# Performance work log

Hardware: AMD Instinct MI355X
Metric: run time of the kernel (lower is better)

## Reference

```python
import jax, jax.numpy as jnp
import numpy as np


def _pad_kernel_like(kernel_oc0, H, W, ks):
    # torch: F.pad(k,(p,p,p,p)) then if shape mismatch F.pad(k,(0,1,0,1))
    p = (H - ks) // 2
    extra = H - (ks + 2 * p)  # 0 or 1
    return jnp.pad(kernel_oc0, ((0, 0), (p, p + extra), (p, p + extra)))


def setup_inputs() -> dict:
    key = jax.random.key(0)
    k1, k2 = jax.random.split(key)
    B, C, H, W = 8, 16, 128, 128
    O, KS = 32, 9
    x = jax.random.normal(k1, (B, C, H, W), dtype=jnp.float32)
    # kaiming_uniform-ish init scale
    fan_in = C * KS * KS
    bound = float(np.sqrt(6.0 / fan_in))
    kernel = jax.random.uniform(k2, (O, C, KS, KS), dtype=jnp.float32,
                                minval=-bound, maxval=bound)
    return {"x": x, "kernel": kernel}


def reference(x, kernel):
    # x: [B,C,H,W] float32, kernel: [O,C,ks,ks] float32
    B, C, H, W = x.shape
    O, ks = kernel.shape[0], kernel.shape[-1]
    # Faithful to original bug: only kernel[:, 0] is used for every input channel.
    k = _pad_kernel_like(kernel[:, 0], H, W, ks)  # [O,H,W]
    # 4f optical FFT convolution: ifftshift -> FFT -> multiply -> IFFT -> fftshift -> |.|
    Fx = jnp.fft.fft2(jnp.fft.ifftshift(x, axes=(-2, -1)))   # [B,C,H,W] complex64
    Fk = jnp.fft.fft2(jnp.fft.ifftshift(k, axes=(-2, -1)))   # [O,H,W]   complex64
    prod = Fx[:, None, :, :, :] * Fk[None, :, None, :, :]    # [B,O,C,H,W]
    field = jnp.fft.fftshift(jnp.fft.ifft2(prod), axes=(-2, -1))
    out_pc = jnp.abs(field)                                  # per-(out,in)-channel intensity
    return out_pc.sum(axis=2)                                # [B,O,H,W]
```

## Files before the change

### kernel.cpp

```cpp
#include <hip/hip_runtime.h>


typedef __attribute__((ext_vector_type(8)))  short  short8;
typedef __attribute__((ext_vector_type(4)))  float  float4v;
typedef __attribute__((ext_vector_type(4)))  unsigned int uint4v;

#define NROW 11
#define NCC  144
#define CHSZ (NROW * NCC)
#define NSLOT (16 * NROW * 72)

__device__ __forceinline__ unsigned short f2bf(float f) {
    union { float f; unsigned int u; } a; a.f = f;
    unsigned int u = a.u;
    u += 0x7fffu + ((u >> 16) & 1u);
    return (unsigned short)(u >> 16);
}

#define MFMA_PHASE(q_, odd_, Bf_, Dv_)                                       \
    {                                                                        \
        uint4v fr;                                                           \
        if (odd_) {                                                          \
            fr.x = (unsigned int)((((unsigned long long)wnd[(q_)+1] << 32) | wnd[(q_)+0]) >> 16); \
            fr.y = (unsigned int)((((unsigned long long)wnd[(q_)+2] << 32) | wnd[(q_)+1]) >> 16); \
            fr.z = (unsigned int)((((unsigned long long)wnd[(q_)+3] << 32) | wnd[(q_)+2]) >> 16); \
            fr.w = (unsigned int)((((unsigned long long)wnd[(q_)+4] << 32) | wnd[(q_)+3]) >> 16); \
        } else {                                                             \
            fr.x = wnd[(q_)+0]; fr.y = wnd[(q_)+1];                          \
            fr.z = wnd[(q_)+2]; fr.w = wnd[(q_)+3];                          \
        }                                                                    \
        short8 af = __builtin_bit_cast(short8, fr);                          \
        Dv_ = __builtin_amdgcn_mfma_f32_16x16x32_bf16(af, Bf_, Dv_, 0, 0, 0); \
    }

#define LOAD_SLOT(s_, v0_, v1_, ad_)                                         \
    {                                                                        \
        int ch  = (s_) / 792;                                                \
        int rem = (s_) - 792 * ch;                                           \
        int rr  = rem / 72;                                                  \
        int ccd = rem - 72 * rr;                                             \
        int cc  = 2 * ccd;                                                   \
        int xrow = (i0 - 4 + rr) & 127;                                      \
        const float* xp = xb + (ch << 14) + (xrow << 7);                     \
        v0_ = xp[(132 - cc) & 127];                                          \
        v1_ = xp[(131 - cc) & 127];                                          \
        ad_ = ch * CHSZ + rr * NCC + cc;                                     \
    }

__global__ __launch_bounds__(512, 4)
void optical_conv_69698729279498(const float* __restrict__ x,
                                 const float* __restrict__ kern,
                                 float* __restrict__ out) {
    __shared__ __align__(16) unsigned short ldsb[16 * CHSZ];

    const int tid = threadIdx.x;
    const int l   = tid & 63;
    const int w   = tid >> 6;
    const int h   = w & 1;
    const int oh  = (w >> 1) & 1;
    const int rh  = w >> 2;
    const int i0  = blockIdx.x * 2;
    const int b   = blockIdx.y;

    const int lk   = l & 15;
    const int g    = (l >> 4) & 1;
    const int hi32 = l >> 5;
    const int g2   = l >> 4;
    const int o    = oh * 16 + lk;

    const float* xb = x + ((size_t)b << 18);

    float v0a[13], v1a[13]; int aa[13];
#pragma unroll
    for (int k = 0; k < 13; ++k) {
        int s = tid + 512 * k;
        LOAD_SLOT(s, v0a[k], v1a[k], aa[k]);
    }
    float v0b[12], v1b[12]; int ab[12];
#pragma unroll
    for (int k = 0; k < 12; ++k) {
        int s = tid + 512 * (13 + k);
        if (s > NSLOT - 1) s = NSLOT - 1;
        LOAD_SLOT(s, v0b[k], v1b[k], ab[k]);
    }
#pragma unroll
    for (int k = 0; k < 13; ++k) {
        unsigned int pk2 = (unsigned int)f2bf(v0a[k]) | ((unsigned int)f2bf(v1a[k]) << 16);
        *(unsigned int*)&ldsb[aa[k]] = pk2;
    }
#pragma unroll
    for (int k = 0; k < 12; ++k) {
        unsigned int pk2 = (unsigned int)f2bf(v0b[k]) | ((unsigned int)f2bf(v1b[k]) << 16);
        *(unsigned int*)&ldsb[ab[k]] = pk2;
    }

    short8 Bf[5];
#pragma unroll
    for (int ck = 0; ck < 5; ++ck) {
        const int ti  = 2 * ck + (g2 >> 1);
        const int tj0 = (g2 & 1) * 8;
        unsigned int pk[4];
#pragma unroll
        for (int ee = 0; ee < 4; ++ee) {
            int tj_a = tj0 + 2 * ee, tj_b = tj_a + 1;
            float va = (ti <= 8 && tj_a <= 8) ? kern[o * 1296 + ti * 9 + tj_a] : 0.f;
            float vb = (ti <= 8 && tj_b <= 8) ? kern[o * 1296 + ti * 9 + tj_b] : 0.f;
            pk[ee] = (unsigned int)f2bf(va) | ((unsigned int)f2bf(vb) << 16);
        }
        uint4v bv; bv.x = pk[0]; bv.y = pk[1]; bv.z = pk[2]; bv.w = pk[3];
        Bf[ck] = __builtin_bit_cast(short8, bv);
    }

    __syncthreads();

    float4v acc[4];
#pragma unroll
    for (int pp = 0; pp < 4; ++pp) acc[pp] = (float4v){0.f, 0.f, 0.f, 0.f};

    for (int c = 0; c < 16; ++c) {
        const unsigned short* lb = ldsb + c * CHSZ;
        float4v D[4];
#pragma unroll
        for (int pp = 0; pp < 4; ++pp) D[pp] = (float4v){0.f, 0.f, 0.f, 0.f};

#pragma unroll
        for (int ck = 0; ck < 5; ++ck) {
            const int ti = 2 * ck + hi32;
            const int r  = 9 - ti + rh;
            const char* base = (const char*)lb + (r * 288 + 240 - 16 * lk + 16 * g);
            uint4v w0 = *(const uint4v*)base;
            uint4v w1 = *(const uint4v*)(base + 16);
            unsigned int wnd[8] = {w0.x, w0.y, w0.z, w0.w, w1.x, w1.y, w1.z, w1.w};
            if (h == 0) {
                MFMA_PHASE(3, 1, Bf[ck], D[0]);
                MFMA_PHASE(3, 0, Bf[ck], D[1]);
                MFMA_PHASE(2, 1, Bf[ck], D[2]);
                MFMA_PHASE(2, 0, Bf[ck], D[3]);
            } else {
                MFMA_PHASE(1, 1, Bf[ck], D[0]);
                MFMA_PHASE(1, 0, Bf[ck], D[1]);
                MFMA_PHASE(0, 1, Bf[ck], D[2]);
                MFMA_PHASE(0, 0, Bf[ck], D[3]);
            }
        }
#pragma unroll
        for (int pp = 0; pp < 4; ++pp)
#pragma unroll
            for (int e = 0; e < 4; ++e) acc[pp][e] += fabsf(D[pp][e]);
    }

    const int i = i0 + rh;
    float* ob = out + ((((size_t)(b * 32 + o)) * 128 + i) << 7);
#pragma unroll
    for (int pp = 0; pp < 4; ++pp) {
        const int pprime = 4 * h + pp;
#pragma unroll
        for (int e = 0; e < 4; ++e)
            ob[32 * g2 + 8 * e + pprime] = acc[pp][e];
    }
}

extern "C" void kernel_launch(void* const* d_in, const int* in_sizes, int n_in,
                              void* d_out, int out_size, void* d_ws, size_t ws_size,
                              hipStream_t stream) {
    const float* x = (const float*)d_in[0];
    const float* kern = (const float*)d_in[1];
    float* out = (float*)d_out;
    dim3 block(512);
    dim3 grid(64, 8);
    hipLaunchKernelGGL(optical_conv_69698729279498, grid, block, 0, stream,
                       x, kern, out);
}
```

Measured before the change: 97.19 us.

## Flatten channel/tap loop and software-pipeline LDS window loads with alignbit fragments

```diff
diff --git a/kernel.cpp b/kernel.cpp
--- a/kernel.cpp
+++ b/kernel.cpp
@@ -17,21 +17,13 @@
     return (unsigned short)(u >> 16);
 }
 
-#define MFMA_PHASE(q_, odd_, Bf_, Dv_)                                       \
-    {                                                                        \
-        uint4v fr;                                                           \
-        if (odd_) {                                                          \
-            fr.x = (unsigned int)((((unsigned long long)wnd[(q_)+1] << 32) | wnd[(q_)+0]) >> 16); \
-            fr.y = (unsigned int)((((unsigned long long)wnd[(q_)+2] << 32) | wnd[(q_)+1]) >> 16); \
-            fr.z = (unsigned int)((((unsigned long long)wnd[(q_)+3] << 32) | wnd[(q_)+2]) >> 16); \
-            fr.w = (unsigned int)((((unsigned long long)wnd[(q_)+4] << 32) | wnd[(q_)+3]) >> 16); \
-        } else {                                                             \
-            fr.x = wnd[(q_)+0]; fr.y = wnd[(q_)+1];                          \
-            fr.z = wnd[(q_)+2]; fr.w = wnd[(q_)+3];                          \
-        }                                                                    \
-        short8 af = __builtin_bit_cast(short8, fr);                          \
-        Dv_ = __builtin_amdgcn_mfma_f32_16x16x32_bf16(af, Bf_, Dv_, 0, 0, 0); \
-    }
+#define FRAG_EVEN(q_) __builtin_bit_cast(short8, (uint4v){                    \
+        wnd[(q_)+0], wnd[(q_)+1], wnd[(q_)+2], wnd[(q_)+3]})
+#define FRAG_ODD(q_)  __builtin_bit_cast(short8, (uint4v){                    \
+        __builtin_amdgcn_alignbit(wnd[(q_)+1], wnd[(q_)+0], 16),              \
+        __builtin_amdgcn_alignbit(wnd[(q_)+2], wnd[(q_)+1], 16),              \
+        __builtin_amdgcn_alignbit(wnd[(q_)+3], wnd[(q_)+2], 16),              \
+        __builtin_amdgcn_alignbit(wnd[(q_)+4], wnd[(q_)+3], 16)})
 
 #define LOAD_SLOT(s_, v0_, v1_, ad_)                                         \
     {                                                                        \
@@ -113,40 +105,54 @@
 
     __syncthreads();
 
+    const char* wbase = (const char*)ldsb
+                      + (240 - 16 * lk + 16 * g) + (9 + rh - hi32) * 288;
+
     float4v acc[4];
 #pragma unroll
     for (int pp = 0; pp < 4; ++pp) acc[pp] = (float4v){0.f, 0.f, 0.f, 0.f};
+    const float4v zero4 = (float4v){0.f, 0.f, 0.f, 0.f};
 
-    for (int c = 0; c < 16; ++c) {
-        const unsigned short* lb = ldsb + c * CHSZ;
-        float4v D[4];
-#pragma unroll
-        for (int pp = 0; pp < 4; ++pp) D[pp] = (float4v){0.f, 0.f, 0.f, 0.f};
+    uint4v bufA[3], bufB[3];
+    float4v D[4];
+
+#define LDWIN(t_, sl_)                                                       \
+    {                                                                        \
+        const char* p_ = wbase + (((t_) / 5) * 3168 - ((t_) % 5) * 576);     \
+        bufA[sl_] = *(const uint4v*)p_;                                      \
+        bufB[sl_] = *(const uint4v*)(p_ + 16);                               \
+    }
+
+    LDWIN(0, 0);
+    LDWIN(1, 1);
 
 #pragma unroll
-        for (int ck = 0; ck < 5; ++ck) {
-            const int ti = 2 * ck + hi32;
-            const int r  = 9 - ti + rh;
-            const char* base = (const char*)lb + (r * 288 + 240 - 16 * lk + 16 * g);
-            uint4v w0 = *(const uint4v*)base;
-            uint4v w1 = *(const uint4v*)(base + 16);
-            unsigned int wnd[8] = {w0.x, w0.y, w0.z, w0.w, w1.x, w1.y, w1.z, w1.w};
-            if (h == 0) {
-                MFMA_PHASE(3, 1, Bf[ck], D[0]);
-                MFMA_PHASE(3, 0, Bf[ck], D[1]);
-                MFMA_PHASE(2, 1, Bf[ck], D[2]);
-                MFMA_PHASE(2, 0, Bf[ck], D[3]);
-            } else {
-                MFMA_PHASE(1, 1, Bf[ck], D[0]);
-                MFMA_PHASE(1, 0, Bf[ck], D[1]);
-                MFMA_PHASE(0, 1, Bf[ck], D[2]);
-                MFMA_PHASE(0, 0, Bf[ck], D[3]);
-            }
+    for (int t = 0; t < 80; ++t) {
+        if (t + 2 < 80) LDWIN(t + 2, (t + 2) % 3);
+        const int ck = t % 5;
+        uint4v w0 = bufA[t % 3], w1 = bufB[t % 3];
+        unsigned int wnd[8] = {w0.x, w0.y, w0.z, w0.w, w1.x, w1.y, w1.z, w1.w};
+        if (h == 0) {
+            short8 f0 = FRAG_ODD(3),  f1 = FRAG_EVEN(3);
+            short8 f2 = FRAG_ODD(2),  f3 = FRAG_EVEN(2);
+            D[0] = __builtin_amdgcn_mfma_f32_16x16x32_bf16(f0, Bf[ck], ck ? D[0] : zero4, 0, 0, 0);
+            D[1] = __builtin_amdgcn_mfma_f32_16x16x32_bf16(f1, Bf[ck], ck ? D[1] : zero4, 0, 0, 0);
+            D[2] = __builtin_amdgcn_mfma_f32_16x16x32_bf16(f2, Bf[ck], ck ? D[2] : zero4, 0, 0, 0);
+            D[3] = __builtin_amdgcn_mfma_f32_16x16x32_bf16(f3, Bf[ck], ck ? D[3] : zero4, 0, 0, 0);
+        } else {
+            short8 f0 = FRAG_ODD(1),  f1 = FRAG_EVEN(1);
+            short8 f2 = FRAG_ODD(0),  f3 = FRAG_EVEN(0);
+            D[0] = __builtin_amdgcn_mfma_f32_16x16x32_bf16(f0, Bf[ck], ck ? D[0] : zero4, 0, 0, 0);
+            D[1] = __builtin_amdgcn_mfma_f32_16x16x32_bf16(f1, Bf[ck], ck ? D[1] : zero4, 0, 0, 0);
+            D[2] = __builtin_amdgcn_mfma_f32_16x16x32_bf16(f2, Bf[ck], ck ? D[2] : zero4, 0, 0, 0);
+            D[3] = __builtin_amdgcn_mfma_f32_16x16x32_bf16(f3, Bf[ck], ck ? D[3] : zero4, 0, 0, 0);
         }
+        if (ck == 4) {
 #pragma unroll
-        for (int pp = 0; pp < 4; ++pp)
+            for (int pp = 0; pp < 4; ++pp)
 #pragma unroll
-            for (int e = 0; e < 4; ++e) acc[pp][e] += fabsf(D[pp][e]);
+                for (int e = 0; e < 4; ++e) acc[pp][e] += fabsf(D[pp][e]);
+        }
     }
 
     const int i = i0 + rh;
```

Measured after the change: 208.9 us. +114.9%, slower.
